# Kernel tuning notes

Hardware: AMD Instinct MI355X
Metric: run time of the kernel (lower is better)

Reference implementation:

```python
import jax, jax.numpy as jnp
import numpy as np

MARGIN = 0.3
LAMBDA_TRIPLET = 1.0
LAMBDA_ID = 1.0
EPS = 1e-6  # torch pairwise_distance eps added to the difference elementwise


def setup_inputs() -> dict:
    key = jax.random.key(0)
    k1, k2 = jax.random.split(key)
    B, N, D = 64, 512, 512
    reid_features = jax.random.normal(k1, (B, N, D), dtype=jnp.float32)
    # ids in [-1, 32): -1 marks invalid detections, as in the torch module
    track_ids = jax.random.randint(k2, (B, N), -1, 32, dtype=jnp.int32)
    return {"reid_features": reid_features, "track_ids": track_ids}


def _tracking_loss(feats, ids, margin):
    B, N, D = feats.shape
    valid = ids >= 0                                   # (B, N)
    same = ids[:, :, None] == ids[:, None, :]          # (B, N, N)
    not_self = ~jnp.eye(N, dtype=bool)                 # (N, N)
    valid_j = valid[:, None, :]                        # candidates must be valid
    pos_mask = same & not_self & valid_j               # (B, N, N)
    neg_mask = (~same) & valid_j                       # (B, N, N)
    has_pos = pos_mask.any(-1)                         # (B, N)
    has_neg = neg_mask.any(-1)
    enough = valid.sum(-1) >= 2                        # (B,)
    anchor_ok = valid & has_pos & has_neg & enough[:, None]
    # torch.nonzero(mask)[0] == first True index -> argmax on bool
    pos_idx = jnp.argmax(pos_mask, axis=-1)            # (B, N)
    neg_idx = jnp.argmax(neg_mask, axis=-1)
    p = jnp.take_along_axis(feats, pos_idx[..., None], axis=1)  # (B, N, D)
    n = jnp.take_along_axis(feats, neg_idx[..., None], axis=1)
    d_ap = jnp.sqrt(jnp.sum((feats - p + EPS) ** 2, axis=-1))   # (B, N)
    d_an = jnp.sqrt(jnp.sum((feats - n + EPS) ** 2, axis=-1))
    per_anchor = jnp.maximum(d_ap - d_an + margin, 0.0)
    num_triplets = anchor_ok.sum()
    total = jnp.sum(per_anchor * anchor_ok.astype(feats.dtype))
    loss = jnp.where(num_triplets > 0,
                     total / jnp.maximum(num_triplets, 1).astype(feats.dtype),
                     jnp.zeros((), feats.dtype))
    return loss * LAMBDA_TRIPLET


def reference(reid_features, track_ids):
    loss_triplet = _tracking_loss(reid_features, track_ids, MARGIN)
    loss_id = jnp.zeros((), reid_features.dtype)
    tracking_loss = loss_triplet + loss_id
    return tracking_loss, loss_triplet, loss_id
```

## Files before the change

kernel.cpp:

```cpp
#include <hip/hip_runtime.h>

#define MARGIN 0.3f
#define EPS 1e-6f

constexpr int B = 64, N = 512, D = 512;
constexpr int NIDS = 32;

constexpr int MB_THREADS = 256;
constexpr int MB_WAVES = MB_THREADS / 64;
constexpr int ANCH_PER_WAVE = 4;
constexpr int MB_BLOCKS = (B * N) / (MB_WAVES * ANCH_PER_WAVE);


__global__ __launch_bounds__(512) void tl_tables(const int* __restrict__ ids,
                                                 int2* __restrict__ desc,
                                                 int2* __restrict__ hdr) {
    __shared__ int s_ids[N];
    __shared__ int s_first[NIDS], s_second[NIDS];
    __shared__ int s_j0, s_jdiff, s_vcnt;
    const int t = threadIdx.x;
    const int b = blockIdx.x;

    if (t < NIDS) { s_first[t] = N; s_second[t] = N; }
    if (t == 0) { s_j0 = N; s_jdiff = N; s_vcnt = 0; }
    __syncthreads();

    const int v = ids[b * N + t];
    s_ids[t] = v;
    if (v >= 0) {
        atomicMin(&s_first[v], t);
        atomicMin(&s_j0, t);
        atomicAdd(&s_vcnt, 1);
    }
    __syncthreads();
    const int id0 = (s_j0 < N) ? s_ids[s_j0] : -2;
    if (v >= 0) {
        if (s_first[v] != t) atomicMin(&s_second[v], t);
        if (v != id0) atomicMin(&s_jdiff, t);
    }
    __syncthreads();

    int2 d = make_int2(-1, -1);
    if (v >= 0 && s_vcnt >= 2) {
        const int posj = (s_first[v] != t) ? s_first[v] : s_second[v];
        const int negj = (v != id0) ? s_j0 : s_jdiff;
        if (posj < N && negj < N) d = make_int2(posj, negj);
    }
    desc[b * N + t] = d;
    if (t == 0) hdr[b] = make_int2(min(s_j0, N - 1), min(s_jdiff, N - 1));
}

__global__ __launch_bounds__(MB_THREADS, 4) void tl_main(const float* __restrict__ feats,
                                                         const int2* __restrict__ desc,
                                                         const int2* __restrict__ hdr,
                                                         float* __restrict__ psum,
                                                         float* __restrict__ pcnt) {
    __shared__ float s_wsum[MB_WAVES];
    __shared__ int s_wcnt[MB_WAVES];

    const int t = threadIdx.x;
    const int lane = t & 63;
    const int wave = t >> 6;
    const int gw = blockIdx.x * MB_WAVES + wave;
    const int b = gw >> 7;
    const int i0 = (gw & 127) * ANCH_PER_WAVE;
    const float* __restrict__ bf = feats + (size_t)b * N * D;

    const int2 h = hdr[b];
    const float4* n0p = (const float4*)(bf + (size_t)h.x * D) + lane * 2;
    const float4* n1p = (const float4*)(bf + (size_t)h.y * D) + lane * 2;
    const float4 n0a = n0p[0], n0b = n0p[1];
    const float4 n1a = n1p[0], n1b = n1p[1];

    float wsum = 0.0f;
    int wcnt = 0;

    #pragma unroll
    for (int k = 0; k < ANCH_PER_WAVE; ++k) {
        const int i = i0 + k;
        const int2 d = desc[b * N + i];
        const bool ok = (d.x >= 0);
        const int pj = ok ? d.x : 0;

        const float4* fa = (const float4*)(bf + (size_t)i * D) + lane * 2;
        const float4* fp = (const float4*)(bf + (size_t)pj * D) + lane * 2;
        const float4 a0 = fa[0], a1 = fa[1];
        const float4 p0 = fp[0], p1 = fp[1];

        const bool useN0 = (d.y == h.x);
        const float4 m0 = useN0 ? n0a : n1a;
        const float4 m1 = useN0 ? n0b : n1b;

        float sap = 0.0f, san = 0.0f, dd;
        dd = a0.x - p0.x + EPS; sap += dd * dd;
        dd = a0.y - p0.y + EPS; sap += dd * dd;
        dd = a0.z - p0.z + EPS; sap += dd * dd;
        dd = a0.w - p0.w + EPS; sap += dd * dd;
        dd = a1.x - p1.x + EPS; sap += dd * dd;
        dd = a1.y - p1.y + EPS; sap += dd * dd;
        dd = a1.z - p1.z + EPS; sap += dd * dd;
        dd = a1.w - p1.w + EPS; sap += dd * dd;
        dd = a0.x - m0.x + EPS; san += dd * dd;
        dd = a0.y - m0.y + EPS; san += dd * dd;
        dd = a0.z - m0.z + EPS; san += dd * dd;
        dd = a0.w - m0.w + EPS; san += dd * dd;
        dd = a1.x - m1.x + EPS; san += dd * dd;
        dd = a1.y - m1.y + EPS; san += dd * dd;
        dd = a1.z - m1.z + EPS; san += dd * dd;
        dd = a1.w - m1.w + EPS; san += dd * dd;

        #pragma unroll
        for (int off = 32; off >= 1; off >>= 1) {
            sap += __shfl_xor(sap, off);
            san += __shfl_xor(san, off);
        }
        const float per = fmaxf(sqrtf(sap) - sqrtf(san) + MARGIN, 0.0f);
        wsum += ok ? per : 0.0f;
        wcnt += ok ? 1 : 0;
    }

    if (lane == 0) { s_wsum[wave] = wsum; s_wcnt[wave] = wcnt; }
    __syncthreads();
    if (t == 0) {
        float s = 0.0f; int c = 0;
        #pragma unroll
        for (int w = 0; w < MB_WAVES; ++w) { s += s_wsum[w]; c += s_wcnt[w]; }
        psum[blockIdx.x] = s;
        pcnt[blockIdx.x] = (float)c;
    }
}

__global__ __launch_bounds__(256) void tl_finalize(const float* __restrict__ psum,
                                                   const float* __restrict__ pcnt,
                                                   float* __restrict__ out) {
    __shared__ float s_s[4], s_c[4];
    const int t = threadIdx.x;
    float s = 0.0f, c = 0.0f;
    for (int k = t; k < MB_BLOCKS; k += 256) { s += psum[k]; c += pcnt[k]; }
    #pragma unroll
    for (int off = 32; off >= 1; off >>= 1) {
        s += __shfl_xor(s, off);
        c += __shfl_xor(c, off);
    }
    if ((t & 63) == 0) { s_s[t >> 6] = s; s_c[t >> 6] = c; }
    __syncthreads();
    if (t == 0) {
        const float S = s_s[0] + s_s[1] + s_s[2] + s_s[3];
        const float C = s_c[0] + s_c[1] + s_c[2] + s_c[3];
        const float loss = (C > 0.0f) ? (S / C) : 0.0f;
        out[0] = loss;
        out[1] = loss;
        out[2] = 0.0f;
    }
}

extern "C" void kernel_launch(void* const* d_in, const int* in_sizes, int n_in,
                              void* d_out, int out_size, void* d_ws, size_t ws_size,
                              hipStream_t stream) {
    const float* feats = (const float*)d_in[0];
    const int* ids = (const int*)d_in[1];
    float* out = (float*)d_out;

    char* ws = (char*)d_ws;
    int2* desc = (int2*)ws;
    int2* hdr = (int2*)(ws + sizeof(int2) * B * N);
    float* psum = (float*)(ws + sizeof(int2) * (B * N + B));
    float* pcnt = psum + MB_BLOCKS;

    tl_tables<<<B, 512, 0, stream>>>(ids, desc, hdr);
    tl_main<<<MB_BLOCKS, MB_THREADS, 0, stream>>>(feats, desc, hdr, psum, pcnt);
    tl_finalize<<<1, 256, 0, stream>>>(psum, pcnt, out);
}
```

Baseline: 104.9 us.

## Batch anchor loads, stage descriptors in LDS, swizzle blocks across XCDs

Each wave now processes 8 anchors in two groups of 4, issuing all anchor and positive row loads for a group before computing, which raises memory-level parallelism. The block's descriptors are staged once into shared memory. Block indices are remapped so consecutive logical segments spread across the 8 XCDs, and the occupancy hint is removed from launch bounds. The valid-count atomics in the table kernel are replaced by a per-wave ballot and popcount. In exchange the kernel uses more registers and launches fewer blocks.

```diff
diff --git a/kernel.cpp b/kernel.cpp
--- a/kernel.cpp
+++ b/kernel.cpp
@@ -8,8 +8,9 @@
 
 constexpr int MB_THREADS = 256;
 constexpr int MB_WAVES = MB_THREADS / 64;
-constexpr int ANCH_PER_WAVE = 4;
-constexpr int MB_BLOCKS = (B * N) / (MB_WAVES * ANCH_PER_WAVE);
+constexpr int ANCH_PER_WAVE = 8;
+constexpr int A_BLOCK = MB_WAVES * ANCH_PER_WAVE;
+constexpr int MB_BLOCKS = (B * N) / A_BLOCK;
 
 
 __global__ __launch_bounds__(512) void tl_tables(const int* __restrict__ ids,
@@ -27,10 +28,11 @@
 
     const int v = ids[b * N + t];
     s_ids[t] = v;
+    const unsigned long long m = __ballot(v >= 0);
+    if ((t & 63) == 0) atomicAdd(&s_vcnt, __popcll(m));
     if (v >= 0) {
         atomicMin(&s_first[v], t);
         atomicMin(&s_j0, t);
-        atomicAdd(&s_vcnt, 1);
     }
     __syncthreads();
     const int id0 = (s_j0 < N) ? s_ids[s_j0] : -2;
@@ -50,21 +52,25 @@
     if (t == 0) hdr[b] = make_int2(min(s_j0, N - 1), min(s_jdiff, N - 1));
 }
 
-__global__ __launch_bounds__(MB_THREADS, 4) void tl_main(const float* __restrict__ feats,
-                                                         const int2* __restrict__ desc,
-                                                         const int2* __restrict__ hdr,
-                                                         float* __restrict__ psum,
-                                                         float* __restrict__ pcnt) {
+__global__ __launch_bounds__(MB_THREADS) void tl_main(const float* __restrict__ feats,
+                                                      const int2* __restrict__ desc,
+                                                      const int2* __restrict__ hdr,
+                                                      float* __restrict__ psum,
+                                                      float* __restrict__ pcnt) {
+    __shared__ int2 s_desc[A_BLOCK];
     __shared__ float s_wsum[MB_WAVES];
     __shared__ int s_wcnt[MB_WAVES];
 
     const int t = threadIdx.x;
     const int lane = t & 63;
     const int wave = t >> 6;
-    const int gw = blockIdx.x * MB_WAVES + wave;
-    const int b = gw >> 7;
-    const int i0 = (gw & 127) * ANCH_PER_WAVE;
+
+    const int logical = ((blockIdx.x & 7) << 7) | (blockIdx.x >> 3);
+    const int b = logical >> 4;
+    const int seg = (logical & 15) * A_BLOCK;
     const float* __restrict__ bf = feats + (size_t)b * N * D;
+
+    if (t < A_BLOCK) s_desc[t] = desc[b * N + seg + t];
 
     const int2 h = hdr[b];
     const float4* n0p = (const float4*)(bf + (size_t)h.x * D) + lane * 2;
@@ -72,51 +78,65 @@
     const float4 n0a = n0p[0], n0b = n0p[1];
     const float4 n1a = n1p[0], n1b = n1p[1];
 
+    __syncthreads();
+
     float wsum = 0.0f;
     int wcnt = 0;
 
     #pragma unroll
-    for (int k = 0; k < ANCH_PER_WAVE; ++k) {
-        const int i = i0 + k;
-        const int2 d = desc[b * N + i];
-        const bool ok = (d.x >= 0);
-        const int pj = ok ? d.x : 0;
+    for (int c = 0; c < ANCH_PER_WAVE / 4; ++c) {
+        const int base = wave * ANCH_PER_WAVE + c * 4;
 
-        const float4* fa = (const float4*)(bf + (size_t)i * D) + lane * 2;
-        const float4* fp = (const float4*)(bf + (size_t)pj * D) + lane * 2;
-        const float4 a0 = fa[0], a1 = fa[1];
-        const float4 p0 = fp[0], p1 = fp[1];
+        int pj[4]; bool okk[4]; bool useN0[4];
+        #pragma unroll
+        for (int k = 0; k < 4; ++k) {
+            const int2 d = s_desc[base + k];
+            okk[k] = (d.x >= 0);
+            pj[k] = okk[k] ? d.x : 0;
+            useN0[k] = (d.y == h.x);
+        }
 
-        const bool useN0 = (d.y == h.x);
-        const float4 m0 = useN0 ? n0a : n1a;
-        const float4 m1 = useN0 ? n0b : n1b;
-
-        float sap = 0.0f, san = 0.0f, dd;
-        dd = a0.x - p0.x + EPS; sap += dd * dd;
-        dd = a0.y - p0.y + EPS; sap += dd * dd;
-        dd = a0.z - p0.z + EPS; sap += dd * dd;
-        dd = a0.w - p0.w + EPS; sap += dd * dd;
-        dd = a1.x - p1.x + EPS; sap += dd * dd;
-        dd = a1.y - p1.y + EPS; sap += dd * dd;
-        dd = a1.z - p1.z + EPS; sap += dd * dd;
-        dd = a1.w - p1.w + EPS; sap += dd * dd;
-        dd = a0.x - m0.x + EPS; san += dd * dd;
-        dd = a0.y - m0.y + EPS; san += dd * dd;
-        dd = a0.z - m0.z + EPS; san += dd * dd;
-        dd = a0.w - m0.w + EPS; san += dd * dd;
-        dd = a1.x - m1.x + EPS; san += dd * dd;
-        dd = a1.y - m1.y + EPS; san += dd * dd;
-        dd = a1.z - m1.z + EPS; san += dd * dd;
-        dd = a1.w - m1.w + EPS; san += dd * dd;
+        float4 A0[4], A1[4], P0[4], P1[4];
+        #pragma unroll
+        for (int k = 0; k < 4; ++k) {
+            const int i = seg + base + k;
+            const float4* fa = (const float4*)(bf + (size_t)i * D) + lane * 2;
+            const float4* fp = (const float4*)(bf + (size_t)pj[k] * D) + lane * 2;
+            A0[k] = fa[0]; A1[k] = fa[1];
+            P0[k] = fp[0]; P1[k] = fp[1];
+        }
 
         #pragma unroll
-        for (int off = 32; off >= 1; off >>= 1) {
-            sap += __shfl_xor(sap, off);
-            san += __shfl_xor(san, off);
+        for (int k = 0; k < 4; ++k) {
+            const float4 m0 = useN0[k] ? n0a : n1a;
+            const float4 m1 = useN0[k] ? n0b : n1b;
+            float sap = 0.0f, san = 0.0f, dd;
+            dd = A0[k].x - P0[k].x + EPS; sap += dd * dd;
+            dd = A0[k].y - P0[k].y + EPS; sap += dd * dd;
+            dd = A0[k].z - P0[k].z + EPS; sap += dd * dd;
+            dd = A0[k].w - P0[k].w + EPS; sap += dd * dd;
+            dd = A1[k].x - P1[k].x + EPS; sap += dd * dd;
+            dd = A1[k].y - P1[k].y + EPS; sap += dd * dd;
+            dd = A1[k].z - P1[k].z + EPS; sap += dd * dd;
+            dd = A1[k].w - P1[k].w + EPS; sap += dd * dd;
+            dd = A0[k].x - m0.x + EPS; san += dd * dd;
+            dd = A0[k].y - m0.y + EPS; san += dd * dd;
+            dd = A0[k].z - m0.z + EPS; san += dd * dd;
+            dd = A0[k].w - m0.w + EPS; san += dd * dd;
+            dd = A1[k].x - m1.x + EPS; san += dd * dd;
+            dd = A1[k].y - m1.y + EPS; san += dd * dd;
+            dd = A1[k].z - m1.z + EPS; san += dd * dd;
+            dd = A1[k].w - m1.w + EPS; san += dd * dd;
+
+            #pragma unroll
+            for (int off = 32; off >= 1; off >>= 1) {
+                sap += __shfl_xor(sap, off);
+                san += __shfl_xor(san, off);
+            }
+            const float per = fmaxf(sqrtf(sap) - sqrtf(san) + MARGIN, 0.0f);
+            wsum += okk[k] ? per : 0.0f;
+            wcnt += okk[k] ? 1 : 0;
         }
-        const float per = fmaxf(sqrtf(sap) - sqrtf(san) + MARGIN, 0.0f);
-        wsum += ok ? per : 0.0f;
-        wcnt += ok ? 1 : 0;
     }
 
     if (lane == 0) { s_wsum[wave] = wsum; s_wcnt[wave] = wcnt; }
```

Result: no change. 105.8 us (+0.9%).
